# Performance work log

Measured on AMD Instinct MI355X. Metric: run time of the kernel, lower is better.

Reference implementation:

```python
import jax, jax.numpy as jnp
import numpy as np

COMMITMENT_COST = 1.0


def setup_inputs() -> dict:
    key = jax.random.key(0)
    k1, k2 = jax.random.split(key)
    x = jax.random.normal(k1, (8, 4096, 256), dtype=jnp.float32)
    codebook = jax.random.normal(k2, (2048, 256), dtype=jnp.float32)
    return {"x": x, "codebook": codebook}


def reference(x, codebook):
    # Squared Euclidean distances via the GEMM expansion:
    # argmin over torch.cdist (sqrt is monotone); dist values are unused.
    x2 = jnp.sum(x * x, axis=-1, keepdims=True)            # [B, T, 1]
    c2 = jnp.sum(codebook * codebook, axis=-1)             # [N]
    d2 = x2 - 2.0 * jnp.einsum('btd,nd->btn', x, codebook) + c2  # [B, T, N]
    indices = jnp.argmin(d2, axis=-1)                      # [B, T]
    codes = codebook[indices]                              # [B, T, D]

    code_loss = jnp.mean((codes - jax.lax.stop_gradient(x)) ** 2)
    embedding_loss = jnp.mean((x - jax.lax.stop_gradient(codes)) ** 2) * COMMITMENT_COST
    loss = code_loss + embedding_loss

    # Straight-through estimator
    quantized = x + jax.lax.stop_gradient(codes - x)
    return quantized, indices, loss
```

## Files before the change

kernel.cpp:

```cpp
#include <hip/hip_runtime.h>

#define D   256
#define BM  64
#define BN  128
#define KC  64

typedef __attribute__((ext_vector_type(8))) short v8s;
typedef __attribute__((ext_vector_type(4))) float v4f;
#define MFMA16 __builtin_amdgcn_mfma_f32_16x16x32_bf16

static __device__ inline unsigned short f2bf(float f) {
    unsigned u = __float_as_uint(f);
    return (unsigned short)((u + 0x7fffu + ((u >> 16) & 1u)) >> 16);
}
static __device__ inline float bf2f(unsigned short s) {
    return __uint_as_float(((unsigned)s) << 16);
}

static __device__ inline void gl_lds16(const unsigned short* g, unsigned short* l) {
    __builtin_amdgcn_global_load_lds(
        (const __attribute__((address_space(1))) unsigned int*)g,
        (__attribute__((address_space(3))) unsigned int*)l, 16, 0, 0);
}

__global__ void vq_prep_c2(const float* __restrict__ cb, float* __restrict__ c2) {
    const int row  = blockIdx.x;
    const int lane = threadIdx.x;
    const float4 v = *reinterpret_cast<const float4*>(cb + (size_t)row * D + lane * 4);
    float s = v.x * v.x + v.y * v.y + v.z * v.z + v.w * v.w;
    #pragma unroll
    for (int off = 32; off > 0; off >>= 1) s += __shfl_down(s, off, 64);
    if (lane == 0) c2[row] = s;
}

__global__ void vq_prep_sw(const float* __restrict__ cb,
                           unsigned short* __restrict__ cbh, unsigned short* __restrict__ cbl) {
    const int chunk = blockIdx.x;
    const int nc = (chunk >> 2) * BN;
    const int kc = (chunk & 3) * KC;
    #pragma unroll
    for (int i = 0; i < 4; ++i) {
        const int p   = i * 256 + threadIdx.x;
        const int seg = p >> 7;
        const int n   = (p & 127) ^ seg;
        const float* src = cb + (size_t)(nc + n) * D + kc + seg * 8;
        const float4 f0 = *reinterpret_cast<const float4*>(src);
        const float4 f1 = *reinterpret_cast<const float4*>(src + 4);
        const float f[8] = {f0.x, f0.y, f0.z, f0.w, f1.x, f1.y, f1.z, f1.w};
        v8s h, l;
        #pragma unroll
        for (int j = 0; j < 8; ++j) {
            unsigned short hb = f2bf(f[j]);
            h[j] = (short)hb;
            l[j] = (short)f2bf(f[j] - bf2f(hb));
        }
        const size_t o = ((size_t)chunk * 1024 + p) * 8;
        *reinterpret_cast<v8s*>(cbh + o) = h;
        *reinterpret_cast<v8s*>(cbl + o) = l;
    }
}

__global__ __launch_bounds__(256, 2) void vq_argmin_mfma(
        const float* __restrict__ x, const float* __restrict__ cb,
        const unsigned short* __restrict__ cbh, const unsigned short* __restrict__ cbl,
        const float* __restrict__ c2, float* __restrict__ idx_out,
        float* __restrict__ qout, float* __restrict__ partial, int N) {
    __shared__ unsigned short lds_h[2][BN * 8 * 8];
    __shared__ unsigned short lds_l[2][BN * 8 * 8];
    __shared__ float red_v[64 * 32];
    __shared__ int   red_i[64 * 32];

    const int tid  = threadIdx.x;
    const int w    = tid >> 6;
    const int lane = tid & 63;
    const int col  = lane & 15;
    const int quad = lane >> 4;
    const int mg   = w >> 1;
    const int ng   = w & 1;
    const int m0   = blockIdx.x * BM;
    const int n_groups = N >> 7;
    const int n_stages = n_groups * 4;

    const unsigned short* gh0 = cbh + ((size_t)(w * 256 + lane)) * 8;
    const unsigned short* gl0 = cbl + ((size_t)(w * 256 + lane)) * 8;

    #pragma unroll
    for (int i = 0; i < 4; ++i) {
        gl_lds16(gh0 + i * 512, &lds_h[0][(w * 256 + i * 64) * 8]);
        gl_lds16(gl0 + i * 512, &lds_l[0][(w * 256 + i * 64) * 8]);
    }

    v8s xh[2][8], xl[2][8];
    #pragma unroll
    for (int mt = 0; mt < 2; ++mt) {
        const float* xr = x + (size_t)(m0 + mg * 32 + mt * 16 + col) * D;
        #pragma unroll
        for (int ks = 0; ks < 8; ++ks) {
            const int kb = ks * 32 + quad * 8;
            const float4 f0 = *reinterpret_cast<const float4*>(xr + kb);
            const float4 f1 = *reinterpret_cast<const float4*>(xr + kb + 4);
            float f[8] = {f0.x, f0.y, f0.z, f0.w, f1.x, f1.y, f1.z, f1.w};
            v8s h, l;
            #pragma unroll
            for (int j = 0; j < 8; ++j) {
                unsigned short hb = f2bf(f[j]);
                h[j] = (short)hb;
                l[j] = (short)f2bf(f[j] - bf2f(hb));
            }
            xh[mt][ks] = h; xl[mt][ks] = l;
        }
    }

    float runmin[2][4];
    int   runidx[2][4];
    #pragma unroll
    for (int mt = 0; mt < 2; ++mt)
        #pragma unroll
        for (int r = 0; r < 4; ++r) { runmin[mt][r] = 3.4e38f; runidx[mt][r] = 0; }

    v4f acc[4][2];
    #pragma unroll
    for (int nt = 0; nt < 4; ++nt)
        #pragma unroll
        for (int mt = 0; mt < 2; ++mt) acc[nt][mt] = 0.0f;

    for (int g = 0; g < n_groups; ++g) {
        #pragma unroll
        for (int cc = 0; cc < 4; ++cc) {
            const int par   = cc & 1;
            const int stage = g * 4 + cc;
            __syncthreads();
            if (stage + 1 < n_stages) {
                const unsigned short* gh = gh0 + (size_t)(stage + 1) * 8192;
                const unsigned short* gl = gl0 + (size_t)(stage + 1) * 8192;
                unsigned short* lh = lds_h[par ^ 1];
                unsigned short* ll = lds_l[par ^ 1];
                #pragma unroll
                for (int i = 0; i < 4; ++i) {
                    gl_lds16(gh + i * 512, lh + (w * 256 + i * 64) * 8);
                    gl_lds16(gl + i * 512, ll + (w * 256 + i * 64) * 8);
                }
            }

            #pragma unroll
            for (int ksk = 0; ksk < 2; ++ksk) {
                const int ks  = cc * 2 + ksk;
                const int seg = ksk * 4 + quad;
                #pragma unroll
                for (int nt = 0; nt < 4; ++nt) {
                    const int p = seg * BN + ((ng * 64 + nt * 16 + col) ^ seg);
                    const v8s ch = *reinterpret_cast<const v8s*>(&lds_h[par][p * 8]);
                    const v8s cl = *reinterpret_cast<const v8s*>(&lds_l[par][p * 8]);
                    #pragma unroll
                    for (int mt = 0; mt < 2; ++mt) {
                        acc[nt][mt] = MFMA16(xh[mt][ks], ch, acc[nt][mt], 0, 0, 0);
                        acc[nt][mt] = MFMA16(xl[mt][ks], ch, acc[nt][mt], 0, 0, 0);
                        acc[nt][mt] = MFMA16(xh[mt][ks], cl, acc[nt][mt], 0, 0, 0);
                    }
                }
            }
        }

        const int nc = g * BN;
        #pragma unroll
        for (int nt = 0; nt < 4; ++nt) {
            const int n   = nc + ng * 64 + nt * 16 + col;
            const float c2n = c2[n];
            #pragma unroll
            for (int mt = 0; mt < 2; ++mt) {
                #pragma unroll
                for (int r = 0; r < 4; ++r) {
                    const float s = c2n - 2.0f * acc[nt][mt][r];
                    if (s < runmin[mt][r]) { runmin[mt][r] = s; runidx[mt][r] = n; }
                }
                acc[nt][mt] = 0.0f;
            }
        }
    }

    __syncthreads();
    #pragma unroll
    for (int mt = 0; mt < 2; ++mt)
        #pragma unroll
        for (int r = 0; r < 4; ++r) {
            const int row  = mg * 32 + mt * 16 + quad * 4 + r;
            const int slot = (ng * 16 + col) ^ (row & 31);
            red_v[row * 32 + slot] = runmin[mt][r];
            red_i[row * 32 + slot] = runidx[mt][r];
        }
    __syncthreads();
    float best = 3.4e38f;
    int   bidx = 0;
    if (tid < 64) {
        #pragma unroll 4
        for (int t = 0; t < 32; ++t) {
            const int  sl = t ^ (tid & 31);
            const float v = red_v[tid * 32 + sl];
            const int  id = red_i[tid * 32 + sl];
            if (v < best || (v == best && id < bidx)) { best = v; bidx = id; }
        }
        idx_out[m0 + tid] = (float)bidx;
    }
    __syncthreads();
    int* idx_sh = reinterpret_cast<int*>(red_v);
    if (tid < 64) idx_sh[tid] = bidx;
    __syncthreads();

    const float* xg2 = x + (size_t)m0 * D;
    float s = 0.0f;
    #pragma unroll
    for (int i = 0; i < 16; ++i) {
        const int g   = i * 256 + tid;
        const int row = g >> 6;
        const int k4  = (g & 63) * 4;
        const int idx = idx_sh[row];
        const float4 c  = *reinterpret_cast<const float4*>(cb  + (size_t)idx * D + k4);
        const float4 xv = *reinterpret_cast<const float4*>(xg2 + (size_t)row * D + k4);
        *reinterpret_cast<float4*>(qout + (size_t)(m0 + row) * D + k4) = c;
        const float dx = c.x - xv.x, dy = c.y - xv.y, dz = c.z - xv.z, dw = c.w - xv.w;
        s += dx * dx + dy * dy + dz * dz + dw * dw;
    }
    #pragma unroll
    for (int off = 32; off > 0; off >>= 1) s += __shfl_down(s, off, 64);
    float* wsum = reinterpret_cast<float*>(red_i);
    if ((tid & 63) == 0) wsum[tid >> 6] = s;
    __syncthreads();
    if (tid == 0) partial[blockIdx.x] = wsum[0] + wsum[1] + wsum[2] + wsum[3];
}

__global__ void vq_reduce_kernel(const float* __restrict__ partial, float* __restrict__ loss,
                                 float scale, int n) {
    __shared__ float red[4];
    const int tid = threadIdx.x;
    float s = 0.0f;
    for (int i = tid; i < n; i += 256) s += partial[i];
    #pragma unroll
    for (int off = 32; off > 0; off >>= 1) s += __shfl_down(s, off, 64);
    if ((tid & 63) == 0) red[tid >> 6] = s;
    __syncthreads();
    if (tid == 0) loss[0] = (red[0] + red[1] + red[2] + red[3]) * scale;
}

extern "C" void kernel_launch(void* const* d_in, const int* in_sizes, int n_in,
                              void* d_out, int out_size, void* d_ws, size_t ws_size,
                              hipStream_t stream) {
    const float* x  = (const float*)d_in[0];
    const float* cb = (const float*)d_in[1];
    const int M = in_sizes[0] / D;
    const int N = in_sizes[1] / D;

    float* qout    = (float*)d_out;
    float* idx_out = qout + (size_t)M * D;
    float* loss    = idx_out + M;

    char* wsb = (char*)d_ws;
    float*          c2      = (float*)wsb;
    unsigned short* cbh     = (unsigned short*)(wsb + 8192);
    unsigned short* cbl     = cbh + (size_t)N * D;
    float*          partial = (float*)(wsb + 8192 + 2 * (size_t)N * D * sizeof(unsigned short));

    vq_prep_c2<<<N, 64, 0, stream>>>(cb, c2);
    vq_prep_sw<<<(N / BN) * (D / KC), 256, 0, stream>>>(cb, cbh, cbl);
    vq_argmin_mfma<<<M / BM, 256, 0, stream>>>(x, cb, cbh, cbl, c2, idx_out, qout, partial, N);
    const float scale = 2.0f / (float)((size_t)M * D);
    vq_reduce_kernel<<<1, 256, 0, stream>>>(partial, loss, scale, M / BM);
}
```

Baseline: 198.3 us.

## Split hi/lo codebook staging into separate barrier phases with vmcnt waits and priorities

Fuses the codebook norm computation into the swizzle prep kernel, which removes one kernel launch. In the main loop, each K-chunk is split into two phases: the hi-part loads and MFMAs, then the lo-part loads and MFMAs. Each phase uses a raw s_barrier with an explicit vmcnt wait instead of __syncthreads, and the MFMA sections are wrapped in s_setprio. The c2 values are prefetched into registers at the start of each group instead of being loaded in the epilogue. This finer-grained overlap adds barriers, and the hand-counted vmcnt values risk racing if the compiler emits other memory ops.

```diff
diff --git a/kernel.cpp b/kernel.cpp
--- a/kernel.cpp
+++ b/kernel.cpp
@@ -9,6 +9,8 @@
 typedef __attribute__((ext_vector_type(4))) float v4f;
 #define MFMA16 __builtin_amdgcn_mfma_f32_16x16x32_bf16
 
+#define WAITVM(N) asm volatile("s_waitcnt vmcnt(" #N ")" ::: "memory")
+
 static __device__ inline unsigned short f2bf(float f) {
     unsigned u = __float_as_uint(f);
     return (unsigned short)((u + 0x7fffu + ((u >> 16) & 1u)) >> 16);
@@ -23,18 +25,9 @@
         (__attribute__((address_space(3))) unsigned int*)l, 16, 0, 0);
 }
 
-__global__ void vq_prep_c2(const float* __restrict__ cb, float* __restrict__ c2) {
-    const int row  = blockIdx.x;
-    const int lane = threadIdx.x;
-    const float4 v = *reinterpret_cast<const float4*>(cb + (size_t)row * D + lane * 4);
-    float s = v.x * v.x + v.y * v.y + v.z * v.z + v.w * v.w;
-    #pragma unroll
-    for (int off = 32; off > 0; off >>= 1) s += __shfl_down(s, off, 64);
-    if (lane == 0) c2[row] = s;
-}
-
 __global__ void vq_prep_sw(const float* __restrict__ cb,
-                           unsigned short* __restrict__ cbh, unsigned short* __restrict__ cbl) {
+                           unsigned short* __restrict__ cbh, unsigned short* __restrict__ cbl,
+                           float* __restrict__ c2) {
     const int chunk = blockIdx.x;
     const int nc = (chunk >> 2) * BN;
     const int kc = (chunk & 3) * KC;
@@ -57,6 +50,17 @@
         const size_t o = ((size_t)chunk * 1024 + p) * 8;
         *reinterpret_cast<v8s*>(cbh + o) = h;
         *reinterpret_cast<v8s*>(cbl + o) = l;
+    }
+    if ((chunk & 3) == 0) {
+        const int w    = threadIdx.x >> 6;
+        const int lane = threadIdx.x & 63;
+        for (int r = w; r < BN; r += 4) {
+            const float4 v = *reinterpret_cast<const float4*>(cb + (size_t)(nc + r) * D + lane * 4);
+            float s = v.x * v.x + v.y * v.y + v.z * v.z + v.w * v.w;
+            #pragma unroll
+            for (int off = 32; off > 0; off >>= 1) s += __shfl_down(s, off, 64);
+            if (lane == 0) c2[nc + r] = s;
+        }
     }
 }
 
@@ -125,23 +129,25 @@
         for (int mt = 0; mt < 2; ++mt) acc[nt][mt] = 0.0f;
 
     for (int g = 0; g < n_groups; ++g) {
+        float c2f[4];
+        #pragma unroll
+        for (int nt = 0; nt < 4; ++nt) c2f[nt] = c2[g * BN + ng * 64 + nt * 16 + col];
+
         #pragma unroll
         for (int cc = 0; cc < 4; ++cc) {
             const int par   = cc & 1;
             const int stage = g * 4 + cc;
-            __syncthreads();
-            if (stage + 1 < n_stages) {
+            const bool more = (stage + 1 < n_stages);
+
+            WAITVM(4);
+            __builtin_amdgcn_s_barrier();
+            if (more) {
                 const unsigned short* gh = gh0 + (size_t)(stage + 1) * 8192;
-                const unsigned short* gl = gl0 + (size_t)(stage + 1) * 8192;
                 unsigned short* lh = lds_h[par ^ 1];
-                unsigned short* ll = lds_l[par ^ 1];
-                #pragma unroll
-                for (int i = 0; i < 4; ++i) {
-                    gl_lds16(gh + i * 512, lh + (w * 256 + i * 64) * 8);
-                    gl_lds16(gl + i * 512, ll + (w * 256 + i * 64) * 8);
-                }
-            }
-
+                #pragma unroll
+                for (int i = 0; i < 4; ++i) gl_lds16(gh + i * 512, lh + (w * 256 + i * 64) * 8);
+            }
+            __builtin_amdgcn_s_setprio(1);
             #pragma unroll
             for (int ksk = 0; ksk < 2; ++ksk) {
                 const int ks  = cc * 2 + ksk;
@@ -150,27 +156,50 @@
                 for (int nt = 0; nt < 4; ++nt) {
                     const int p = seg * BN + ((ng * 64 + nt * 16 + col) ^ seg);
                     const v8s ch = *reinterpret_cast<const v8s*>(&lds_h[par][p * 8]);
-                    const v8s cl = *reinterpret_cast<const v8s*>(&lds_l[par][p * 8]);
                     #pragma unroll
                     for (int mt = 0; mt < 2; ++mt) {
                         acc[nt][mt] = MFMA16(xh[mt][ks], ch, acc[nt][mt], 0, 0, 0);
                         acc[nt][mt] = MFMA16(xl[mt][ks], ch, acc[nt][mt], 0, 0, 0);
-                        acc[nt][mt] = MFMA16(xh[mt][ks], cl, acc[nt][mt], 0, 0, 0);
                     }
                 }
             }
+            __builtin_amdgcn_s_setprio(0);
+
+            if (more) { WAITVM(4); }
+            else      { WAITVM(0); }
+            __builtin_amdgcn_s_barrier();
+            if (more) {
+                const unsigned short* gl = gl0 + (size_t)(stage + 1) * 8192;
+                unsigned short* ll = lds_l[par ^ 1];
+                #pragma unroll
+                for (int i = 0; i < 4; ++i) gl_lds16(gl + i * 512, ll + (w * 256 + i * 64) * 8);
+            }
+            __builtin_amdgcn_s_setprio(1);
+            #pragma unroll
+            for (int ksk = 0; ksk < 2; ++ksk) {
+                const int ks  = cc * 2 + ksk;
+                const int seg = ksk * 4 + quad;
+                #pragma unroll
+                for (int nt = 0; nt < 4; ++nt) {
+                    const int p = seg * BN + ((ng * 64 + nt * 16 + col) ^ seg);
+                    const v8s cl = *reinterpret_cast<const v8s*>(&lds_l[par][p * 8]);
+                    #pragma unroll
+                    for (int mt = 0; mt < 2; ++mt)
+                        acc[nt][mt] = MFMA16(xh[mt][ks], cl, acc[nt][mt], 0, 0, 0);
+                }
+            }
+            __builtin_amdgcn_s_setprio(0);
         }
 
         const int nc = g * BN;
         #pragma unroll
         for (int nt = 0; nt < 4; ++nt) {
-            const int n   = nc + ng * 64 + nt * 16 + col;
-            const float c2n = c2[n];
+            const int n = nc + ng * 64 + nt * 16 + col;
             #pragma unroll
             for (int mt = 0; mt < 2; ++mt) {
                 #pragma unroll
                 for (int r = 0; r < 4; ++r) {
-                    const float s = c2n - 2.0f * acc[nt][mt][r];
+                    const float s = c2f[nt] - 2.0f * acc[nt][mt][r];
                     if (s < runmin[mt][r]) { runmin[mt][r] = s; runidx[mt][r] = n; }
                 }
                 acc[nt][mt] = 0.0f;
@@ -259,8 +288,7 @@
     unsigned short* cbl     = cbh + (size_t)N * D;
     float*          partial = (float*)(wsb + 8192 + 2 * (size_t)N * D * sizeof(unsigned short));
 
-    vq_prep_c2<<<N, 64, 0, stream>>>(cb, c2);
-    vq_prep_sw<<<(N / BN) * (D / KC), 256, 0, stream>>>(cb, cbh, cbl);
+    vq_prep_sw<<<(N / BN) * (D / KC), 256, 0, stream>>>(cb, cbh, cbl, c2);
     vq_argmin_mfma<<<M / BM, 256, 0, stream>>>(x, cb, cbh, cbl, c2, idx_out, qout, partial, N);
     const float scale = 2.0f / (float)((size_t)M * D);
     vq_reduce_kernel<<<1, 256, 0, stream>>>(partial, loss, scale, M / BM);
```

Measured after the change: 204.6 us. 1.03x slower.

## Switch to 32x32x16 MFMA tiles with fine-grained barriers and LDS-cached c2

Applied to the files above, without the earlier changes.

Replaces the 16x16x32 bf16 MFMA tiling with 32x32x16 MFMAs, so each warp handles a 32x64 tile with two 16-float accumulators. The aim is fewer LDS fragment reads per FLOP and higher MFMA throughput per instruction. It also replaces __syncthreads with raw s_barrier plus explicit vmcnt waits around the double-buffered global-to-LDS loads, raises wave priority during the MFMA section, and stages c2 in shared memory. In exchange, the reduction buffers are aliased onto the codebook LDS, register pressure from 16-entry running min/idx arrays goes up, and correctness now depends on the hand-counted vmcnt values.

```diff
diff --git a/kernel.cpp b/kernel.cpp
--- a/kernel.cpp
+++ b/kernel.cpp
@@ -5,9 +5,12 @@
 #define BN  128
 #define KC  64
 
-typedef __attribute__((ext_vector_type(8))) short v8s;
-typedef __attribute__((ext_vector_type(4))) float v4f;
-#define MFMA16 __builtin_amdgcn_mfma_f32_16x16x32_bf16
+typedef __attribute__((ext_vector_type(8)))  short v8s;
+typedef __attribute__((ext_vector_type(4)))  float v4f;
+typedef __attribute__((ext_vector_type(16))) float v16f;
+#define MFMA32 __builtin_amdgcn_mfma_f32_32x32x16_bf16
+
+#define WAITVM(N) asm volatile("s_waitcnt vmcnt(" #N ")" ::: "memory")
 
 static __device__ inline unsigned short f2bf(float f) {
     unsigned u = __float_as_uint(f);
@@ -67,14 +70,13 @@
         float* __restrict__ qout, float* __restrict__ partial, int N) {
     __shared__ unsigned short lds_h[2][BN * 8 * 8];
     __shared__ unsigned short lds_l[2][BN * 8 * 8];
-    __shared__ float red_v[64 * 32];
-    __shared__ int   red_i[64 * 32];
+    __shared__ float c2s[2048];
 
     const int tid  = threadIdx.x;
     const int w    = tid >> 6;
     const int lane = tid & 63;
-    const int col  = lane & 15;
-    const int quad = lane >> 4;
+    const int l31  = lane & 31;
+    const int hi   = lane >> 5;
     const int mg   = w >> 1;
     const int ng   = w & 1;
     const int m0   = blockIdx.x * BM;
@@ -90,13 +92,22 @@
         gl_lds16(gl0 + i * 512, &lds_l[0][(w * 256 + i * 64) * 8]);
     }
 
-    v8s xh[2][8], xl[2][8];
-    #pragma unroll
-    for (int mt = 0; mt < 2; ++mt) {
-        const float* xr = x + (size_t)(m0 + mg * 32 + mt * 16 + col) * D;
-        #pragma unroll
-        for (int ks = 0; ks < 8; ++ks) {
-            const int kb = ks * 32 + quad * 8;
+    {
+        const int o = tid * 8;
+        if (o < N) {
+            const float4 a = *reinterpret_cast<const float4*>(c2 + o);
+            const float4 b = *reinterpret_cast<const float4*>(c2 + o + 4);
+            *reinterpret_cast<float4*>(&c2s[o])     = a;
+            *reinterpret_cast<float4*>(&c2s[o + 4]) = b;
+        }
+    }
+
+    v8s xh[16], xl[16];
+    {
+        const float* xr = x + (size_t)(m0 + mg * 32 + l31) * D;
+        #pragma unroll
+        for (int ks = 0; ks < 16; ++ks) {
+            const int kb = ks * 16 + hi * 8;
             const float4 f0 = *reinterpret_cast<const float4*>(xr + kb);
             const float4 f1 = *reinterpret_cast<const float4*>(xr + kb + 4);
             float f[8] = {f0.x, f0.y, f0.z, f0.w, f1.x, f1.y, f1.z, f1.w};
@@ -107,30 +118,38 @@
                 h[j] = (short)hb;
                 l[j] = (short)f2bf(f[j] - bf2f(hb));
             }
-            xh[mt][ks] = h; xl[mt][ks] = l;
-        }
-    }
-
-    float runmin[2][4];
-    int   runidx[2][4];
-    #pragma unroll
-    for (int mt = 0; mt < 2; ++mt)
-        #pragma unroll
-        for (int r = 0; r < 4; ++r) { runmin[mt][r] = 3.4e38f; runidx[mt][r] = 0; }
-
-    v4f acc[4][2];
-    #pragma unroll
-    for (int nt = 0; nt < 4; ++nt)
-        #pragma unroll
-        for (int mt = 0; mt < 2; ++mt) acc[nt][mt] = 0.0f;
+            xh[ks] = h; xl[ks] = l;
+        }
+    }
+
+    unsigned aoff[4][2];
+    #pragma unroll
+    for (int ksl = 0; ksl < 4; ++ksl) {
+        const int seg = ksl * 2 + hi;
+        #pragma unroll
+        for (int nt = 0; nt < 2; ++nt)
+            aoff[ksl][nt] = (unsigned)((seg * 128 + ((ng * 64 + nt * 32 + l31) ^ seg)) * 16);
+    }
+
+    float runmin[16];
+    int   runidx[16];
+    #pragma unroll
+    for (int r = 0; r < 16; ++r) { runmin[r] = 3.4e38f; runidx[r] = 0; }
+
+    v16f acc[2];
+    acc[0] = 0.0f; acc[1] = 0.0f;
+
+    __syncthreads();
 
     for (int g = 0; g < n_groups; ++g) {
         #pragma unroll
         for (int cc = 0; cc < 4; ++cc) {
             const int par   = cc & 1;
             const int stage = g * 4 + cc;
-            __syncthreads();
-            if (stage + 1 < n_stages) {
+            const bool more = (stage + 1 < n_stages);
+
+            __builtin_amdgcn_s_barrier();
+            if (more) {
                 const unsigned short* gh = gh0 + (size_t)(stage + 1) * 8192;
                 const unsigned short* gl = gl0 + (size_t)(stage + 1) * 8192;
                 unsigned short* lh = lds_h[par ^ 1];
@@ -140,69 +159,68 @@
                     gl_lds16(gh + i * 512, lh + (w * 256 + i * 64) * 8);
                     gl_lds16(gl + i * 512, ll + (w * 256 + i * 64) * 8);
                 }
-            }
-
+                WAITVM(8);
+            } else {
+                WAITVM(0);
+            }
+            __builtin_amdgcn_s_barrier();
+
+            __builtin_amdgcn_s_setprio(1);
             #pragma unroll
-            for (int ksk = 0; ksk < 2; ++ksk) {
-                const int ks  = cc * 2 + ksk;
-                const int seg = ksk * 4 + quad;
+            for (int ksl = 0; ksl < 4; ++ksl) {
+                const int ks = cc * 4 + ksl;
                 #pragma unroll
-                for (int nt = 0; nt < 4; ++nt) {
-                    const int p = seg * BN + ((ng * 64 + nt * 16 + col) ^ seg);
-                    const v8s ch = *reinterpret_cast<const v8s*>(&lds_h[par][p * 8]);
-                    const v8s cl = *reinterpret_cast<const v8s*>(&lds_l[par][p * 8]);
-                    #pragma unroll
-                    for (int mt = 0; mt < 2; ++mt) {
-                        acc[nt][mt] = MFMA16(xh[mt][ks], ch, acc[nt][mt], 0, 0, 0);
-                        acc[nt][mt] = MFMA16(xl[mt][ks], ch, acc[nt][mt], 0, 0, 0);
-                        acc[nt][mt] = MFMA16(xh[mt][ks], cl, acc[nt][mt], 0, 0, 0);
-                    }
+                for (int nt = 0; nt < 2; ++nt) {
+                    const v8s ch = *reinterpret_cast<const v8s*>(
+                        reinterpret_cast<const char*>(&lds_h[par][0]) + aoff[ksl][nt]);
+                    const v8s cl = *reinterpret_cast<const v8s*>(
+                        reinterpret_cast<const char*>(&lds_l[par][0]) + aoff[ksl][nt]);
+                    acc[nt] = MFMA32(xh[ks], ch, acc[nt], 0, 0, 0);
+                    acc[nt] = MFMA32(xl[ks], ch, acc[nt], 0, 0, 0);
+                    acc[nt] = MFMA32(xh[ks], cl, acc[nt], 0, 0, 0);
                 }
             }
-        }
-
-        const int nc = g * BN;
-        #pragma unroll
-        for (int nt = 0; nt < 4; ++nt) {
-            const int n   = nc + ng * 64 + nt * 16 + col;
-            const float c2n = c2[n];
+            __builtin_amdgcn_s_setprio(0);
+        }
+
+        #pragma unroll
+        for (int nt = 0; nt < 2; ++nt) {
+            const int n = g * 128 + ng * 64 + nt * 32 + l31;
+            const float c2n = c2s[n];
             #pragma unroll
-            for (int mt = 0; mt < 2; ++mt) {
-                #pragma unroll
-                for (int r = 0; r < 4; ++r) {
-                    const float s = c2n - 2.0f * acc[nt][mt][r];
-                    if (s < runmin[mt][r]) { runmin[mt][r] = s; runidx[mt][r] = n; }
-                }
-                acc[nt][mt] = 0.0f;
-            }
-        }
-    }
-
-    __syncthreads();
-    #pragma unroll
-    for (int mt = 0; mt < 2; ++mt)
-        #pragma unroll
-        for (int r = 0; r < 4; ++r) {
-            const int row  = mg * 32 + mt * 16 + quad * 4 + r;
-            const int slot = (ng * 16 + col) ^ (row & 31);
-            red_v[row * 32 + slot] = runmin[mt][r];
-            red_i[row * 32 + slot] = runidx[mt][r];
-        }
+            for (int r = 0; r < 16; ++r) {
+                const float s = c2n - 2.0f * acc[nt][r];
+                if (s < runmin[r]) { runmin[r] = s; runidx[r] = n; }
+            }
+            acc[nt] = 0.0f;
+        }
+    }
+
+    __syncthreads();
+    float* red_v = reinterpret_cast<float*>(&lds_h[0][0]);
+    int*   red_i = reinterpret_cast<int*>(&lds_h[1][0]);
+    #pragma unroll
+    for (int r = 0; r < 16; ++r) {
+        const int row  = mg * 32 + (r & 3) + 8 * (r >> 2) + 4 * hi;
+        const int slot = (ng * 32 + l31) ^ row;
+        red_v[row * 64 + slot] = runmin[r];
+        red_i[row * 64 + slot] = runidx[r];
+    }
     __syncthreads();
     float best = 3.4e38f;
     int   bidx = 0;
     if (tid < 64) {
         #pragma unroll 4
-        for (int t = 0; t < 32; ++t) {
-            const int  sl = t ^ (tid & 31);
-            const float v = red_v[tid * 32 + sl];
-            const int  id = red_i[tid * 32 + sl];
+        for (int t = 0; t < 64; ++t) {
+            const int  sl = t ^ tid;
+            const float v = red_v[tid * 64 + sl];
+            const int  id = red_i[tid * 64 + sl];
             if (v < best || (v == best && id < bidx)) { best = v; bidx = id; }
         }
         idx_out[m0 + tid] = (float)bidx;
     }
     __syncthreads();
-    int* idx_sh = reinterpret_cast<int*>(red_v);
+    int* idx_sh = reinterpret_cast<int*>(&lds_h[0][0]);
     if (tid < 64) idx_sh[tid] = bidx;
     __syncthreads();
 
@@ -210,9 +228,9 @@
     float s = 0.0f;
     #pragma unroll
     for (int i = 0; i < 16; ++i) {
-        const int g   = i * 256 + tid;
-        const int row = g >> 6;
-        const int k4  = (g & 63) * 4;
+        const int gix = i * 256 + tid;
+        const int row = gix >> 6;
+        const int k4  = (gix & 63) * 4;
         const int idx = idx_sh[row];
         const float4 c  = *reinterpret_cast<const float4*>(cb  + (size_t)idx * D + k4);
         const float4 xv = *reinterpret_cast<const float4*>(xg2 + (size_t)row * D + k4);
@@ -222,7 +240,7 @@
     }
     #pragma unroll
     for (int off = 32; off > 0; off >>= 1) s += __shfl_down(s, off, 64);
-    float* wsum = reinterpret_cast<float*>(red_i);
+    float* wsum = reinterpret_cast<float*>(&lds_l[0][0]);
     if ((tid & 63) == 0) wsum[tid >> 6] = s;
     __syncthreads();
     if (tid == 0) partial[blockIdx.x] = wsum[0] + wsum[1] + wsum[2] + wsum[3];
```

Measured after the change: 208.9 us. +5.3%, slower.

## Deepen codebook LDS pipeline to 4-slot ring with finer stages and atomic loss

Applied to the files above, without the earlier changes.

Replaces the double-buffered 64-K LDS staging with a 4-slot ring of 32-K stages, prefetched two stages ahead and throttled with explicit vmcnt waits and raw s_barrier, and raises wave priority around the MFMA bursts. The c2 norms are cached in LDS, and the separate reduce kernel is dropped in favour of an atomicAdd into a loss zeroed by the prep kernel. The prep swizzle kernel is split into four times as many blocks. The main loop is hardcoded for N=2048 (31+1 superblocks), so it no longer adapts to other codebook sizes, and atomic float accumulation makes the loss summation order nondeterministic.

```diff
diff --git a/kernel.cpp b/kernel.cpp
--- a/kernel.cpp
+++ b/kernel.cpp
@@ -3,11 +3,13 @@
 #define D   256
 #define BM  64
 #define BN  128
-#define KC  64
+#define NSTAGES 128
 
 typedef __attribute__((ext_vector_type(8))) short v8s;
 typedef __attribute__((ext_vector_type(4))) float v4f;
 #define MFMA16 __builtin_amdgcn_mfma_f32_16x16x32_bf16
+
+#define WAITVM(N) asm volatile("s_waitcnt vmcnt(" #N ")" ::: "memory")
 
 static __device__ inline unsigned short f2bf(float f) {
     unsigned u = __float_as_uint(f);
@@ -23,9 +25,11 @@
         (__attribute__((address_space(3))) unsigned int*)l, 16, 0, 0);
 }
 
-__global__ void vq_prep_c2(const float* __restrict__ cb, float* __restrict__ c2) {
+__global__ void vq_prep_c2(const float* __restrict__ cb, float* __restrict__ c2,
+                           float* __restrict__ loss) {
     const int row  = blockIdx.x;
     const int lane = threadIdx.x;
+    if (row == 0 && lane == 0) loss[0] = 0.0f;
     const float4 v = *reinterpret_cast<const float4*>(cb + (size_t)row * D + lane * 4);
     float s = v.x * v.x + v.y * v.y + v.z * v.z + v.w * v.w;
     #pragma unroll
@@ -35,40 +39,36 @@
 
 __global__ void vq_prep_sw(const float* __restrict__ cb,
                            unsigned short* __restrict__ cbh, unsigned short* __restrict__ cbl) {
-    const int chunk = blockIdx.x;
+    const int b     = blockIdx.x;
+    const int chunk = b >> 2;
     const int nc = (chunk >> 2) * BN;
-    const int kc = (chunk & 3) * KC;
-    #pragma unroll
-    for (int i = 0; i < 4; ++i) {
-        const int p   = i * 256 + threadIdx.x;
-        const int seg = p >> 7;
-        const int n   = (p & 127) ^ seg;
-        const float* src = cb + (size_t)(nc + n) * D + kc + seg * 8;
-        const float4 f0 = *reinterpret_cast<const float4*>(src);
-        const float4 f1 = *reinterpret_cast<const float4*>(src + 4);
-        const float f[8] = {f0.x, f0.y, f0.z, f0.w, f1.x, f1.y, f1.z, f1.w};
-        v8s h, l;
-        #pragma unroll
-        for (int j = 0; j < 8; ++j) {
-            unsigned short hb = f2bf(f[j]);
-            h[j] = (short)hb;
-            l[j] = (short)f2bf(f[j] - bf2f(hb));
-        }
-        const size_t o = ((size_t)chunk * 1024 + p) * 8;
-        *reinterpret_cast<v8s*>(cbh + o) = h;
-        *reinterpret_cast<v8s*>(cbl + o) = l;
-    }
+    const int kc = (chunk & 3) * 64;
+    const int p   = (b & 3) * 256 + threadIdx.x;
+    const int seg = p >> 7;
+    const int n   = (p & 127) ^ seg;
+    const float* src = cb + (size_t)(nc + n) * D + kc + seg * 8;
+    const float4 f0 = *reinterpret_cast<const float4*>(src);
+    const float4 f1 = *reinterpret_cast<const float4*>(src + 4);
+    const float f[8] = {f0.x, f0.y, f0.z, f0.w, f1.x, f1.y, f1.z, f1.w};
+    v8s h, l;
+    #pragma unroll
+    for (int j = 0; j < 8; ++j) {
+        unsigned short hb = f2bf(f[j]);
+        h[j] = (short)hb;
+        l[j] = (short)f2bf(f[j] - bf2f(hb));
+    }
+    const size_t o = ((size_t)chunk * 1024 + p) * 8;
+    *reinterpret_cast<v8s*>(cbh + o) = h;
+    *reinterpret_cast<v8s*>(cbl + o) = l;
 }
 
 __global__ __launch_bounds__(256, 2) void vq_argmin_mfma(
         const float* __restrict__ x, const float* __restrict__ cb,
         const unsigned short* __restrict__ cbh, const unsigned short* __restrict__ cbl,
         const float* __restrict__ c2, float* __restrict__ idx_out,
-        float* __restrict__ qout, float* __restrict__ partial, int N) {
-    __shared__ unsigned short lds_h[2][BN * 8 * 8];
-    __shared__ unsigned short lds_l[2][BN * 8 * 8];
-    __shared__ float red_v[64 * 32];
-    __shared__ int   red_i[64 * 32];
+        float* __restrict__ qout, float* __restrict__ loss, float scale, int N) {
+    __shared__ unsigned short ring[4][8192];
+    __shared__ float c2s[2048];
 
     const int tid  = threadIdx.x;
     const int w    = tid >> 6;
@@ -78,16 +78,31 @@
     const int mg   = w >> 1;
     const int ng   = w & 1;
     const int m0   = blockIdx.x * BM;
-    const int n_groups = N >> 7;
-    const int n_stages = n_groups * 4;
-
-    const unsigned short* gh0 = cbh + ((size_t)(w * 256 + lane)) * 8;
-    const unsigned short* gl0 = cbl + ((size_t)(w * 256 + lane)) * 8;
-
-    #pragma unroll
-    for (int i = 0; i < 4; ++i) {
-        gl_lds16(gh0 + i * 512, &lds_h[0][(w * 256 + i * 64) * 8]);
-        gl_lds16(gl0 + i * 512, &lds_l[0][(w * 256 + i * 64) * 8]);
+
+    const unsigned short* gh0 = cbh + ((size_t)(w * 128 + lane)) * 8;
+    const unsigned short* gl0 = cbl + ((size_t)(w * 128 + lane)) * 8;
+
+    {
+        unsigned short* d0 = &ring[0][0] + w * 1024;
+        unsigned short* d1 = &ring[1][0] + w * 1024;
+        gl_lds16(gh0,              d0);
+        gl_lds16(gh0 + 512,        d0 + 512);
+        gl_lds16(gl0,              d0 + 4096);
+        gl_lds16(gl0 + 512,        d0 + 4096 + 512);
+        gl_lds16(gh0 + 4096,       d1);
+        gl_lds16(gh0 + 4096 + 512, d1 + 512);
+        gl_lds16(gl0 + 4096,       d1 + 4096);
+        gl_lds16(gl0 + 4096 + 512, d1 + 4096 + 512);
+    }
+
+    {
+        const int o = tid * 8;
+        if (o < N) {
+            const float4 a = *reinterpret_cast<const float4*>(c2 + o);
+            const float4 b = *reinterpret_cast<const float4*>(c2 + o + 4);
+            *reinterpret_cast<float4*>(&c2s[o])     = a;
+            *reinterpret_cast<float4*>(&c2s[o + 4]) = b;
+        }
     }
 
     v8s xh[2][8], xl[2][8];
@@ -111,6 +126,14 @@
         }
     }
 
+    unsigned offA[4], offB[4];
+    #pragma unroll
+    for (int nt = 0; nt < 4; ++nt) {
+        const int n = ng * 64 + nt * 16 + col;
+        offA[nt] = (unsigned)((quad * 128 + (n ^ quad)) * 16);
+        offB[nt] = offA[nt] ^ 64;
+    }
+
     float runmin[2][4];
     int   runidx[2][4];
     #pragma unroll
@@ -124,61 +147,84 @@
         #pragma unroll
         for (int mt = 0; mt < 2; ++mt) acc[nt][mt] = 0.0f;
 
-    for (int g = 0; g < n_groups; ++g) {
-        #pragma unroll
-        for (int cc = 0; cc < 4; ++cc) {
-            const int par   = cc & 1;
-            const int stage = g * 4 + cc;
-            __syncthreads();
-            if (stage + 1 < n_stages) {
-                const unsigned short* gh = gh0 + (size_t)(stage + 1) * 8192;
-                const unsigned short* gl = gl0 + (size_t)(stage + 1) * 8192;
-                unsigned short* lh = lds_h[par ^ 1];
-                unsigned short* ll = lds_l[par ^ 1];
-                #pragma unroll
-                for (int i = 0; i < 4; ++i) {
-                    gl_lds16(gh + i * 512, lh + (w * 256 + i * 64) * 8);
-                    gl_lds16(gl + i * 512, ll + (w * 256 + i * 64) * 8);
-                }
-            }
-
-            #pragma unroll
-            for (int ksk = 0; ksk < 2; ++ksk) {
-                const int ks  = cc * 2 + ksk;
-                const int seg = ksk * 4 + quad;
-                #pragma unroll
-                for (int nt = 0; nt < 4; ++nt) {
-                    const int p = seg * BN + ((ng * 64 + nt * 16 + col) ^ seg);
-                    const v8s ch = *reinterpret_cast<const v8s*>(&lds_h[par][p * 8]);
-                    const v8s cl = *reinterpret_cast<const v8s*>(&lds_l[par][p * 8]);
-                    #pragma unroll
-                    for (int mt = 0; mt < 2; ++mt) {
-                        acc[nt][mt] = MFMA16(xh[mt][ks], ch, acc[nt][mt], 0, 0, 0);
-                        acc[nt][mt] = MFMA16(xl[mt][ks], ch, acc[nt][mt], 0, 0, 0);
-                        acc[nt][mt] = MFMA16(xh[mt][ks], cl, acc[nt][mt], 0, 0, 0);
-                    }
-                }
-            }
-        }
-
-        const int nc = g * BN;
-        #pragma unroll
-        for (int nt = 0; nt < 4; ++nt) {
-            const int n   = nc + ng * 64 + nt * 16 + col;
-            const float c2n = c2[n];
-            #pragma unroll
-            for (int mt = 0; mt < 2; ++mt) {
-                #pragma unroll
-                for (int r = 0; r < 4; ++r) {
-                    const float s = c2n - 2.0f * acc[nt][mt][r];
-                    if (s < runmin[mt][r]) { runmin[mt][r] = s; runidx[mt][r] = n; }
-                }
-                acc[nt][mt] = 0.0f;
-            }
-        }
-    }
-
-    __syncthreads();
+    __syncthreads();
+
+#define STAGE(U, KS0, ISSUE, WVM)                                              \
+    {                                                                          \
+        WAITVM(WVM);                                                           \
+        __builtin_amdgcn_s_barrier();                                          \
+        if (!(ISSUE)) __builtin_amdgcn_sched_barrier(0);                       \
+        if (ISSUE) {                                                           \
+            const int s2 = stage_base + (U) + 2;                               \
+            const unsigned short* gh = gh0 + (size_t)s2 * 4096;                \
+            const unsigned short* gl = gl0 + (size_t)s2 * 4096;                \
+            unsigned short* dst = &ring[((U) + 2) & 3][0] + w * 1024;          \
+            gl_lds16(gh,       dst);                                           \
+            gl_lds16(gh + 512, dst + 512);                                     \
+            gl_lds16(gl,       dst + 4096);                                    \
+            gl_lds16(gl + 512, dst + 4096 + 512);                              \
+        }                                                                      \
+        __builtin_amdgcn_s_setprio(1);                                         \
+        {                                                                      \
+            const char* cbase = (const char*)&ring[(U) & 3][0];                \
+            _Pragma("unroll")                                                  \
+            for (int nt = 0; nt < 4; ++nt) {                                   \
+                const unsigned off = ((U) & 1) ? offB[nt] : offA[nt];          \
+                const v8s ch = *reinterpret_cast<const v8s*>(cbase + off);     \
+                const v8s cl = *reinterpret_cast<const v8s*>(cbase + 8192 + off); \
+                acc[nt][0] = MFMA16(xh[0][(KS0) + (U)], ch, acc[nt][0], 0, 0, 0); \
+                acc[nt][1] = MFMA16(xh[1][(KS0) + (U)], ch, acc[nt][1], 0, 0, 0); \
+                acc[nt][0] = MFMA16(xl[0][(KS0) + (U)], ch, acc[nt][0], 0, 0, 0); \
+                acc[nt][1] = MFMA16(xl[1][(KS0) + (U)], ch, acc[nt][1], 0, 0, 0); \
+                acc[nt][0] = MFMA16(xh[0][(KS0) + (U)], cl, acc[nt][0], 0, 0, 0); \
+                acc[nt][1] = MFMA16(xh[1][(KS0) + (U)], cl, acc[nt][1], 0, 0, 0); \
+            }                                                                  \
+        }                                                                      \
+        __builtin_amdgcn_s_setprio(0);                                         \
+    }
+
+#define FINALIZE(G)                                                            \
+    {                                                                          \
+        const int g_ = (G);                                                    \
+        _Pragma("unroll")                                                      \
+        for (int nt = 0; nt < 4; ++nt) {                                       \
+            const int n = g_ * 128 + ng * 64 + nt * 16 + col;                  \
+            const float c2n = c2s[n];                                          \
+            _Pragma("unroll")                                                  \
+            for (int mt = 0; mt < 2; ++mt) {                                   \
+                _Pragma("unroll")                                              \
+                for (int r = 0; r < 4; ++r) {                                  \
+                    const float sv = c2n - 2.0f * acc[nt][mt][r];              \
+                    if (sv < runmin[mt][r]) { runmin[mt][r] = sv; runidx[mt][r] = n; } \
+                }                                                              \
+                acc[nt][mt] = 0.0f;                                            \
+            }                                                                  \
+        }                                                                      \
+    }
+
+    for (int sb = 0; sb < 31; ++sb) {
+        const int stage_base = sb * 4;
+        if ((sb & 1) == 0) {
+            STAGE(0, 0, 1, 4) STAGE(1, 0, 1, 4) STAGE(2, 0, 1, 4) STAGE(3, 0, 1, 4)
+        } else {
+            STAGE(0, 4, 1, 4) STAGE(1, 4, 1, 4) STAGE(2, 4, 1, 4) STAGE(3, 4, 1, 4)
+            FINALIZE(sb >> 1)
+        }
+    }
+    {
+        const int stage_base = 124;
+        STAGE(0, 4, 1, 4)
+        STAGE(1, 4, 1, 4)
+        STAGE(2, 4, 0, 4)
+        STAGE(3, 4, 0, 0)
+        FINALIZE(15)
+    }
+#undef STAGE
+#undef FINALIZE
+
+    __syncthreads();
+    float* red_v = reinterpret_cast<float*>(&ring[0][0]);
+    int*   red_i = reinterpret_cast<int*>(&ring[1][0]);
     #pragma unroll
     for (int mt = 0; mt < 2; ++mt)
         #pragma unroll
@@ -202,7 +248,7 @@
         idx_out[m0 + tid] = (float)bidx;
     }
     __syncthreads();
-    int* idx_sh = reinterpret_cast<int*>(red_v);
+    int* idx_sh = reinterpret_cast<int*>(&ring[2][0]);
     if (tid < 64) idx_sh[tid] = bidx;
     __syncthreads();
 
@@ -210,9 +256,9 @@
     float s = 0.0f;
     #pragma unroll
     for (int i = 0; i < 16; ++i) {
-        const int g   = i * 256 + tid;
-        const int row = g >> 6;
-        const int k4  = (g & 63) * 4;
+        const int gix = i * 256 + tid;
+        const int row = gix >> 6;
+        const int k4  = (gix & 63) * 4;
         const int idx = idx_sh[row];
         const float4 c  = *reinterpret_cast<const float4*>(cb  + (size_t)idx * D + k4);
         const float4 xv = *reinterpret_cast<const float4*>(xg2 + (size_t)row * D + k4);
@@ -222,23 +268,10 @@
     }
     #pragma unroll
     for (int off = 32; off > 0; off >>= 1) s += __shfl_down(s, off, 64);
-    float* wsum = reinterpret_cast<float*>(red_i);
+    float* wsum = reinterpret_cast<float*>(&ring[3][0]);
     if ((tid & 63) == 0) wsum[tid >> 6] = s;
     __syncthreads();
-    if (tid == 0) partial[blockIdx.x] = wsum[0] + wsum[1] + wsum[2] + wsum[3];
-}
-
-__global__ void vq_reduce_kernel(const float* __restrict__ partial, float* __restrict__ loss,
-                                 float scale, int n) {
-    __shared__ float red[4];
-    const int tid = threadIdx.x;
-    float s = 0.0f;
-    for (int i = tid; i < n; i += 256) s += partial[i];
-    #pragma unroll
-    for (int off = 32; off > 0; off >>= 1) s += __shfl_down(s, off, 64);
-    if ((tid & 63) == 0) red[tid >> 6] = s;
-    __syncthreads();
-    if (tid == 0) loss[0] = (red[0] + red[1] + red[2] + red[3]) * scale;
+    if (tid == 0) atomicAdd(loss, (wsum[0] + wsum[1] + wsum[2] + wsum[3]) * scale);
 }
 
 extern "C" void kernel_launch(void* const* d_in, const int* in_sizes, int n_in,
@@ -254,14 +287,13 @@
     float* loss    = idx_out + M;
 
     char* wsb = (char*)d_ws;
-    float*          c2      = (float*)wsb;
-    unsigned short* cbh     = (unsigned short*)(wsb + 8192);
-    unsigned short* cbl     = cbh + (size_t)N * D;
-    float*          partial = (float*)(wsb + 8192 + 2 * (size_t)N * D * sizeof(unsigned short));
-
-    vq_prep_c2<<<N, 64, 0, stream>>>(cb, c2);
-    vq_prep_sw<<<(N / BN) * (D / KC), 256, 0, stream>>>(cb, cbh, cbl);
-    vq_argmin_mfma<<<M / BM, 256, 0, stream>>>(x, cb, cbh, cbl, c2, idx_out, qout, partial, N);
+    float*          c2  = (float*)wsb;
+    unsigned short* cbh = (unsigned short*)(wsb + 8192);
+    unsigned short* cbl = cbh + (size_t)N * D;
+
+    vq_prep_c2<<<N, 64, 0, stream>>>(cb, c2, loss);
+    vq_prep_sw<<<(N / BN) * 4 * 4, 256, 0, stream>>>(cb, cbh, cbl);
     const float scale = 2.0f / (float)((size_t)M * D);
-    vq_reduce_kernel<<<1, 256, 0, stream>>>(partial, loss, scale, M / BM);
-}
+    vq_argmin_mfma<<<M / BM, 256, 0, stream>>>(x, cb, cbh, cbl, c2, idx_out, qout,
+                                               loss, scale, N);
+}
```

After: 224.5 us. 13.2% more time.
